# Optimization experiments

Hardware: AMD Instinct MI355X
Metric: run time of the kernel (lower is better)

Reference implementation:

```python
import jax, jax.numpy as jnp
import numpy as np

B, LQ, C = 4, 4096, 384
NH, NL, NP = 6, 1, 4
HL, WL = 64, 64
LV = HL * WL
DH = C // NH
EPS = 1e-6


def layer_norm(x, g, b):
    mu = jnp.mean(x, axis=-1, keepdims=True)
    var = jnp.mean(jnp.square(x - mu), axis=-1, keepdims=True)
    return (x - mu) * jax.lax.rsqrt(var + EPS) * g + b


def ms_deform_attn_core(value, spatial_shapes, level_start_index, loc, attn_w):
    # value [B,LV,NH,DH]; loc [B,LQ,NH,NL,NP,2] in [0,1]; attn_w [B,LQ,NH,NL,NP]
    ss = np.asarray(spatial_shapes)
    lsi = np.asarray(level_start_index)
    Bv, _, nH, dh = value.shape
    Lq = loc.shape[1]
    nP = loc.shape[4]
    out = jnp.zeros((Bv, Lq, nH, dh), value.dtype)
    for l in range(loc.shape[3]):
        Hl, Wl = int(ss[l, 0]), int(ss[l, 1])
        st = int(lsi[l])
        vflat = value[:, st:st + Hl * Wl]  # [B, Hl*Wl, nH, dh]
        xy = loc[:, :, :, l]               # [B,LQ,nH,NP,2]
        # grid_sample(align_corners=False): pixel = loc * size - 0.5
        x = xy[..., 0] * Wl - 0.5
        y = xy[..., 1] * Hl - 0.5
        x0 = jnp.floor(x)
        y0 = jnp.floor(y)
        wx = x - x0
        wy = y - y0
        x0i = x0.astype(jnp.int32)
        y0i = y0.astype(jnp.int32)

        def gather(xi, yi):
            # zero padding outside the feature map (padding_mode='zeros')
            valid = (xi >= 0) & (xi < Wl) & (yi >= 0) & (yi < Hl)
            idx = jnp.clip(yi, 0, Hl - 1) * Wl + jnp.clip(xi, 0, Wl - 1)  # [B,LQ,nH,NP]
            idx2 = idx.transpose(0, 1, 3, 2).reshape(Bv, Lq * nP, nH)
            g = jnp.take_along_axis(vflat, idx2[..., None], axis=1)       # [B,LQ*NP,nH,dh]
            g = g.reshape(Bv, Lq, nP, nH, dh).transpose(0, 1, 3, 2, 4)    # [B,LQ,nH,NP,dh]
            return g * valid[..., None].astype(value.dtype)

        samp = (gather(x0i, y0i) * ((1 - wx) * (1 - wy))[..., None]
                + gather(x0i + 1, y0i) * (wx * (1 - wy))[..., None]
                + gather(x0i, y0i + 1) * ((1 - wx) * wy)[..., None]
                + gather(x0i + 1, y0i + 1) * (wx * wy)[..., None])
        out = out + jnp.einsum('bqhpd,bqhp->bqhd', samp, attn_w[:, :, :, l])
    return out.reshape(Bv, Lq, nH * dh)


def setup_inputs() -> dict:
    key = jax.random.key(0)
    ks = jax.random.split(key, 12)
    s = 0.02
    return {
        'query': jax.random.normal(ks[0], (B, LQ, C), jnp.float32),
        'reference_points': jax.random.uniform(ks[1], (B, LQ, NL, 2), dtype=jnp.float32),
        'feat': jax.random.normal(ks[2], (B, LV, C), jnp.float32),
        'spatial_shapes': jnp.array([[HL, WL]], jnp.int32),
        'level_start_index': jnp.array([0], jnp.int32),
        'ln_q_g': jnp.ones((C,), jnp.float32), 'ln_q_b': jnp.zeros((C,), jnp.float32),
        'ln_f_g': jnp.ones((C,), jnp.float32), 'ln_f_b': jnp.zeros((C,), jnp.float32),
        'gamma': jax.random.normal(ks[3], (C,), jnp.float32) * 0.1,
        'Wv': jax.random.normal(ks[4], (C, C), jnp.float32) * s,
        'bv': jnp.zeros((C,), jnp.float32),
        'Wo': jax.random.normal(ks[5], (C, NH * NL * NP * 2), jnp.float32) * s,
        'bo': jax.random.normal(ks[6], (NH * NL * NP * 2,), jnp.float32) * 0.5,
        'Wa': jax.random.normal(ks[7], (C, NH * NL * NP), jnp.float32) * s,
        'ba': jnp.zeros((NH * NL * NP,), jnp.float32),
        'Wout': jax.random.normal(ks[8], (C, C), jnp.float32) * s,
        'bout': jnp.zeros((C,), jnp.float32),
    }


def reference(query, reference_points, feat, spatial_shapes, level_start_index,
              ln_q_g, ln_q_b, ln_f_g, ln_f_b, gamma,
              Wv, bv, Wo, bo, Wa, ba, Wout, bout):
    q = layer_norm(query, ln_q_g, ln_q_b)
    f = layer_norm(feat, ln_f_g, ln_f_b)
    value = (f @ Wv + bv).reshape(B, LV, NH, DH)
    offsets = (q @ Wo + bo).reshape(B, LQ, NH, NL, NP, 2)
    attn_w = jax.nn.softmax((q @ Wa + ba).reshape(B, LQ, NH, NL * NP), axis=-1)
    attn_w = attn_w.reshape(B, LQ, NH, NL, NP)
    # offset normalizer is (W, H) per level
    norm = jnp.stack([spatial_shapes[:, 1], spatial_shapes[:, 0]], -1).astype(jnp.float32)
    loc = reference_points[:, :, None, :, None, :] + offsets / norm[None, None, None, :, None, :]
    attn = ms_deform_attn_core(value, spatial_shapes, level_start_index, loc, attn_w)
    attn = attn @ Wout + bout
    return query + gamma * attn
```

## Files before the change

kernel.cpp:

```cpp
#include <hip/hip_runtime.h>
#include <math.h>

#define B_    4
#define LQ_   4096
#define C_    384
#define NH_   6
#define NP_   4
#define HL_   64
#define WL_   64
#define LV_   (HL_ * WL_)
#define ROWS_ (B_ * LQ_)
#define EPS_  1e-6f
#define NOFF_ 48
#define NLOG_ 24
#define WCTR_ 128

typedef unsigned short u16;
typedef unsigned int   u32;
typedef __bf16 bf16x8 __attribute__((ext_vector_type(8)));
typedef float  f32x4  __attribute__((ext_vector_type(4)));

__device__ __forceinline__ u16 f2bf(float f) {
    u32 u = __float_as_uint(f);
    u += 0x7fff + ((u >> 16) & 1);
    return (u16)(u >> 16);
}
__device__ __forceinline__ u32 pack2bf(float a, float b) {
    return (u32)f2bf(a) | ((u32)f2bf(b) << 16);
}

__device__ __forceinline__ f32x4 mfma16(bf16x8 a, bf16x8 b, f32x4 c) {
    return __builtin_amdgcn_mfma_f32_16x16x32_bf16(a, b, c, 0, 0, 0);
}

__device__ __forceinline__ void gl_lds16(const u16* g, u16* l) {
    __builtin_amdgcn_global_load_lds(
        (const __attribute__((address_space(1))) unsigned int*)g,
        (__attribute__((address_space(3))) unsigned int*)l, 16, 0, 0);
}

__device__ __forceinline__ void vm_wait4() { asm volatile("s_waitcnt vmcnt(4)" ::: "memory"); }
__device__ __forceinline__ void vm_wait0() { asm volatile("s_waitcnt vmcnt(0)" ::: "memory"); }
__device__ __forceinline__ void lgkm0()    { asm volatile("s_waitcnt lgkmcnt(0)" ::: "memory"); }
__device__ __forceinline__ void barrier_() { asm volatile("s_barrier" ::: "memory"); }

#define LN_BLOCKS_   8192
#define PREP_BLOCKS_ 1345

__global__ __launch_bounds__(256) void ln_prep(
    const float* __restrict__ query, const float* __restrict__ feat,
    const float* __restrict__ qg, const float* __restrict__ qbv,
    const float* __restrict__ fg, const float* __restrict__ fbv,
    u16* __restrict__ qout, u16* __restrict__ fout,
    const float* __restrict__ Wv, const float* __restrict__ Wout,
    const float* __restrict__ Wo, const float* __restrict__ Wa,
    const float* __restrict__ bo, const float* __restrict__ ba,
    u16* __restrict__ WvT, u16* __restrict__ WoutT, u16* __restrict__ WcT,
    float* __restrict__ bias_c)
{
    if (blockIdx.x < LN_BLOCKS_) {
        int wid  = threadIdx.x >> 6;
        int lane = threadIdx.x & 63;
        int row  = blockIdx.x * 4 + wid;
        const float *src, *g, *bsh;
        u16* dst;
        int r;
        if (row < ROWS_) { src = query; g = qg; bsh = qbv; dst = qout; r = row; }
        else             { src = feat;  g = fg; bsh = fbv; dst = fout; r = row - ROWS_; }

        const float* x = src + (size_t)r * C_;
        float4 a4 = *(const float4*)(x + 4 * lane);
        float2 a2 = *(const float2*)(x + 256 + 2 * lane);
        float v0 = a4.x, v1 = a4.y, v2 = a4.z, v3 = a4.w, v4 = a2.x, v5 = a2.y;

        float s = v0 + v1 + v2 + v3 + v4 + v5;
#pragma unroll
        for (int off = 32; off; off >>= 1) s += __shfl_xor(s, off);
        float mu = s * (1.f / C_);

        float d0 = v0 - mu, d1 = v1 - mu, d2 = v2 - mu;
        float d3 = v3 - mu, d4 = v4 - mu, d5 = v5 - mu;
        float s2 = d0*d0 + d1*d1 + d2*d2 + d3*d3 + d4*d4 + d5*d5;
#pragma unroll
        for (int off = 32; off; off >>= 1) s2 += __shfl_xor(s2, off);
        float rs = rsqrtf(s2 * (1.f / C_) + EPS_);

        float4 g4 = *(const float4*)(g + 4 * lane);
        float4 b4 = *(const float4*)(bsh + 4 * lane);
        float2 g2 = *(const float2*)(g + 256 + 2 * lane);
        float2 b2 = *(const float2*)(bsh + 256 + 2 * lane);

        float o0 = d0 * rs * g4.x + b4.x;
        float o1 = d1 * rs * g4.y + b4.y;
        float o2 = d2 * rs * g4.z + b4.z;
        float o3 = d3 * rs * g4.w + b4.w;
        float o4 = d4 * rs * g2.x + b2.x;
        float o5 = d5 * rs * g2.y + b2.y;

        u16* y = dst + (size_t)r * C_;
        uint2 w0; w0.x = pack2bf(o0, o1); w0.y = pack2bf(o2, o3);
        *(uint2*)(y + 4 * lane) = w0;
        *(u32*)(y + 256 + 2 * lane) = pack2bf(o4, o5);
    } else {
        const int KN = 384 * 384;
        int idx = (blockIdx.x - LN_BLOCKS_) * 256 + threadIdx.x;
        if (idx < KN) {
            int n = idx / 384, k = idx - n * 384;
            WvT[idx] = f2bf(Wv[k * 384 + n]);
        } else if (idx < 2 * KN) {
            int t = idx - KN;
            int n = t / 384, k = t - n * 384;
            WoutT[t] = f2bf(Wout[k * 384 + n]);
        } else if (idx < 2 * KN + WCTR_ * 384) {
            int t = idx - 2 * KN;
            int n = t / 384, k = t - n * 384;
            float v = (n < 48) ? Wo[k * 48 + n] : (n < 72 ? Wa[k * 24 + (n - 48)] : 0.f);
            WcT[t] = f2bf(v);
        } else if (idx < 2 * KN + WCTR_ * 384 + 80) {
            int n = idx - (2 * KN + WCTR_ * 384);
            bias_c[n] = (n < 48) ? bo[n] : (n < 72 ? ba[n - 48] : 0.f);
        }
    }
}

__global__ __launch_bounds__(256) void gemm_combined(
    const u16* __restrict__ fb, const u16* __restrict__ qb,
    const u16* __restrict__ WvT, const u16* __restrict__ WcT,
    const float* __restrict__ bv, const float* __restrict__ bias_c,
    u16* __restrict__ valb, float* __restrict__ offs, float* __restrict__ logits)
{
    __shared__ __align__(16) u16 As_[2][4096];
    __shared__ __align__(16) u16 Bs_[2][4096];

    int g    = blockIdx.x;
    int tid  = threadIdx.x;
    int lane = tid & 63, wid = tid >> 6;
    int fr = lane & 15, quad = lane >> 4;

    int srow = tid >> 2;
    int scol = (tid & 3) * 8;

    if (g < 384) {
        int m0 = (g & 127) * 128, n0 = (g >> 7) * 128;
        const u16* aSrc = fb  + (size_t)(m0 + srow) * 384 + scol;
        const u16* bSrc = WvT + (size_t)(n0 + srow) * 384 + scol;

        int wm = (wid >> 1) * 64, wn = (wid & 1) * 64;

        f32x4 zero = {0.f, 0.f, 0.f, 0.f};
        f32x4 acc[4][4];
#pragma unroll
        for (int i = 0; i < 4; ++i)
#pragma unroll
            for (int j = 0; j < 4; ++j) acc[i][j] = zero;

#define STGV(bu, t) { \
            gl_lds16(aSrc + (t)*32,            &As_[bu][tid*8]); \
            gl_lds16(aSrc + 64*384 + (t)*32,   &As_[bu][tid*8 + 2048]); \
            gl_lds16(bSrc + (t)*32,            &Bs_[bu][tid*8]); \
            gl_lds16(bSrc + 64*384 + (t)*32,   &Bs_[bu][tid*8 + 2048]); }

        STGV(0, 0)
        STGV(1, 1)
#pragma unroll
        for (int t = 0; t < 12; ++t) {
            const int bu = t & 1;
            if (t < 11) vm_wait4(); else vm_wait0();
            barrier_();
            bf16x8 af[4], bfr[4];
#pragma unroll
            for (int i = 0; i < 4; ++i) {
                af[i]  = *(const bf16x8*)&As_[bu][(wm + i * 16 + fr) * 32 + quad * 8];
                bfr[i] = *(const bf16x8*)&Bs_[bu][(wn + i * 16 + fr) * 32 + quad * 8];
            }
            lgkm0();
            barrier_();
            if (t < 10) STGV(bu, t + 2)
#pragma unroll
            for (int i = 0; i < 4; ++i)
#pragma unroll
                for (int j = 0; j < 4; ++j)
                    acc[i][j] = mfma16(af[i], bfr[j], acc[i][j]);
        }
#undef STGV

#pragma unroll
        for (int i = 0; i < 4; ++i) {
            int row = m0 + wm + i * 16 + quad * 4;
#pragma unroll
            for (int j = 0; j < 4; ++j) {
                int col = n0 + wn + j * 16 + fr;
                float bcol = bv[col];
#pragma unroll
                for (int r = 0; r < 4; ++r)
                    valb[(size_t)(row + r) * C_ + col] = f2bf(acc[i][j][r] + bcol);
            }
        }
    } else {
        int m0 = (g - 384) * 128;
        const u16* aSrc = qb  + (size_t)(m0 + srow) * 384 + scol;
        const u16* bSrc = WcT + (size_t)srow * 384 + scol;

        int wm = wid * 32;

        f32x4 zero = {0.f, 0.f, 0.f, 0.f};
        f32x4 acc[2][5];
#pragma unroll
        for (int i = 0; i < 2; ++i)
#pragma unroll
            for (int j = 0; j < 5; ++j) acc[i][j] = zero;

#define STGS(bu, t) { \
            gl_lds16(aSrc + (t)*32,            &As_[bu][tid*8]); \
            gl_lds16(aSrc + 64*384 + (t)*32,   &As_[bu][tid*8 + 2048]); \
            gl_lds16(bSrc + (t)*32,            &Bs_[bu][tid*8]); \
            gl_lds16(bSrc + 64*384 + (t)*32,   &Bs_[bu][tid*8 + 2048]); }

        STGS(0, 0)
        STGS(1, 1)
#pragma unroll
        for (int t = 0; t < 12; ++t) {
            const int bu = t & 1;
            if (t < 11) vm_wait4(); else vm_wait0();
            barrier_();
            bf16x8 af[2], bfr[5];
#pragma unroll
            for (int i = 0; i < 2; ++i)
                af[i] = *(const bf16x8*)&As_[bu][(wm + i * 16 + fr) * 32 + quad * 8];
#pragma unroll
            for (int j = 0; j < 5; ++j)
                bfr[j] = *(const bf16x8*)&Bs_[bu][(j * 16 + fr) * 32 + quad * 8];
            lgkm0();
            barrier_();
            if (t < 10) STGS(bu, t + 2)
#pragma unroll
            for (int i = 0; i < 2; ++i)
#pragma unroll
                for (int j = 0; j < 5; ++j)
                    acc[i][j] = mfma16(af[i], bfr[j], acc[i][j]);
        }
#undef STGS

#pragma unroll
        for (int i = 0; i < 2; ++i) {
            int row = m0 + wm + i * 16 + quad * 4;
#pragma unroll
            for (int j = 0; j < 5; ++j) {
                int col = j * 16 + fr;
                if (col < 72) {
                    float bcol = bias_c[col];
#pragma unroll
                    for (int r = 0; r < 4; ++r) {
                        float v = acc[i][j][r] + bcol;
                        if (col < 48) offs[(size_t)(row + r) * NOFF_ + col] = v;
                        else          logits[(size_t)(row + r) * NLOG_ + (col - 48)] = v;
                    }
                }
            }
        }
    }
}

__global__ __launch_bounds__(384) void sampler(
    const u16*  __restrict__ value,
    const float* __restrict__ rp,
    const float* __restrict__ offs,
    const float* __restrict__ logits,
    u16* __restrict__ attn)
{
    int t = threadIdx.x;
    int g = blockIdx.x;
    int b     = (g & 7) >> 1;
    int local = ((g >> 3) << 1) | (g & 1);
    int q  = t / 48, dc = t - q * 48;
    int h  = dc >> 3;
    int col0 = dc << 3;
    int r  = b * LQ_ + local * 8 + q;

    float4 lg  = *(const float4*)(logits + (size_t)r * NLOG_ + h * 4);
    float2 rpv = *(const float2*)(rp + (size_t)r * 2);
    float4 of0 = *(const float4*)(offs + (size_t)r * NOFF_ + h * 8);
    float4 of1 = *(const float4*)(offs + (size_t)r * NOFF_ + h * 8 + 4);

    float mx = fmaxf(fmaxf(lg.x, lg.y), fmaxf(lg.z, lg.w));
    float e0 = __expf(lg.x - mx), e1 = __expf(lg.y - mx);
    float e2 = __expf(lg.z - mx), e3 = __expf(lg.w - mx);
    float rden = 1.f / (e0 + e1 + e2 + e3);
    float aws[4] = {e0 * rden, e1 * rden, e2 * rden, e3 * rden};
    float oxs[4] = {of0.x, of0.z, of1.x, of1.z};
    float oys[4] = {of0.y, of0.w, of1.y, of1.w};

    const u16* vbase = value + (size_t)b * LV_ * C_ + col0;
    float acc[8] = {0.f, 0.f, 0.f, 0.f, 0.f, 0.f, 0.f, 0.f};
#pragma unroll
    for (int p = 0; p < NP_; ++p) {
        float x = rpv.x * (float)WL_ + oxs[p] - 0.5f;
        float y = rpv.y * (float)HL_ + oys[p] - 0.5f;
        float x0f = floorf(x), y0f = floorf(y);
        float wx = x - x0f, wy = y - y0f;
        int x0 = (int)x0f, y0 = (int)y0f;
#pragma unroll
        for (int c = 0; c < 4; ++c) {
            int xi = x0 + (c & 1);
            int yi = y0 + (c >> 1);
            bool valid = (xi >= 0) && (xi < WL_) && (yi >= 0) && (yi < HL_);
            int xc = xi < 0 ? 0 : (xi > WL_ - 1 ? WL_ - 1 : xi);
            int yc = yi < 0 ? 0 : (yi > HL_ - 1 ? HL_ - 1 : yi);
            float w = ((c & 1) ? wx : 1.f - wx) * ((c >> 1) ? wy : 1.f - wy) * aws[p];
            w = valid ? w : 0.f;
            bf16x8 vv = *(const bf16x8*)(vbase + (size_t)(yc * WL_ + xc) * C_);
#pragma unroll
            for (int e = 0; e < 8; ++e) acc[e] += w * (float)vv[e];
        }
    }

    uint4 o;
    o.x = pack2bf(acc[0], acc[1]);
    o.y = pack2bf(acc[2], acc[3]);
    o.z = pack2bf(acc[4], acc[5]);
    o.w = pack2bf(acc[6], acc[7]);
    *(uint4*)(attn + (size_t)r * C_ + col0) = o;
}

__global__ __launch_bounds__(256) void out_gemm(
    const u16* __restrict__ A, const u16* __restrict__ Bt,
    const float* __restrict__ bout, const float* __restrict__ gamma,
    const float* __restrict__ query, float* __restrict__ out)
{
    __shared__ __align__(16) u16 As_[2][4096];
    __shared__ __align__(16) u16 Bs_[2][4096];

    int g    = blockIdx.x;
    int tid  = threadIdx.x;
    int lane = tid & 63, wid = tid >> 6;
    int fr = lane & 15, quad = lane >> 4;

    int srow = tid >> 2;
    int scol = (tid & 3) * 8;

    int m0 = (g & 127) * 128, n0 = (g >> 7) * 96;
    const u16* aSrc = A  + (size_t)(m0 + srow) * 384 + scol;
    const u16* bSrc = Bt + (size_t)(n0 + srow) * 384 + scol;

    int wm = (wid >> 1) * 64, wn = (wid & 1) * 48;

    f32x4 zero = {0.f, 0.f, 0.f, 0.f};
    f32x4 acc[4][3];
#pragma unroll
    for (int i = 0; i < 4; ++i)
#pragma unroll
        for (int j = 0; j < 3; ++j) acc[i][j] = zero;

#define STGO(bu, t) { \
        gl_lds16(aSrc + (t)*32,            &As_[bu][tid*8]); \
        gl_lds16(aSrc + 64*384 + (t)*32,   &As_[bu][tid*8 + 2048]); \
        gl_lds16(bSrc + (t)*32,            &Bs_[bu][tid*8]); \
        gl_lds16(bSrc + 64*384 + (t)*32,   &Bs_[bu][tid*8 + 2048]); }

    STGO(0, 0)
    STGO(1, 1)
#pragma unroll
    for (int t = 0; t < 12; ++t) {
        const int bu = t & 1;
        if (t < 11) vm_wait4(); else vm_wait0();
        barrier_();
        bf16x8 af[4], bfr[3];
#pragma unroll
        for (int i = 0; i < 4; ++i)
            af[i] = *(const bf16x8*)&As_[bu][(wm + i * 16 + fr) * 32 + quad * 8];
#pragma unroll
        for (int j = 0; j < 3; ++j)
            bfr[j] = *(const bf16x8*)&Bs_[bu][(wn + j * 16 + fr) * 32 + quad * 8];
        lgkm0();
        barrier_();
        if (t < 10) STGO(bu, t + 2)
#pragma unroll
        for (int i = 0; i < 4; ++i)
#pragma unroll
            for (int j = 0; j < 3; ++j)
                acc[i][j] = mfma16(af[i], bfr[j], acc[i][j]);
    }
#undef STGO

#pragma unroll
    for (int i = 0; i < 4; ++i) {
        int row = m0 + wm + i * 16 + quad * 4;
#pragma unroll
        for (int j = 0; j < 3; ++j) {
            int col = n0 + wn + j * 16 + fr;
            float bc = bout[col], gm = gamma[col];
#pragma unroll
            for (int r = 0; r < 4; ++r) {
                size_t o = (size_t)(row + r) * C_ + col;
                out[o] = query[o] + gm * (acc[i][j][r] + bc);
            }
        }
    }
}

extern "C" void kernel_launch(void* const* d_in, const int* in_sizes, int n_in,
                              void* d_out, int out_size, void* d_ws, size_t ws_size,
                              hipStream_t stream)
{
    const float* query  = (const float*)d_in[0];
    const float* rp     = (const float*)d_in[1];
    const float* feat   = (const float*)d_in[2];
    const float* gamma  = (const float*)d_in[9];
    const float* Wv     = (const float*)d_in[10];
    const float* bv     = (const float*)d_in[11];
    const float* Wo     = (const float*)d_in[12];
    const float* bo     = (const float*)d_in[13];
    const float* Wa     = (const float*)d_in[14];
    const float* ba     = (const float*)d_in[15];
    const float* Wout   = (const float*)d_in[16];
    const float* bout   = (const float*)d_in[17];
    float* out = (float*)d_out;

    u16* wsu    = (u16*)d_ws;
    u16* qb     = wsu;
    u16* fb     = qb    + (size_t)ROWS_ * C_;
    u16* valb   = fb    + (size_t)ROWS_ * C_;
    u16* attnb  = valb  + (size_t)ROWS_ * C_;
    u16* WvT    = attnb + (size_t)ROWS_ * C_;
    u16* WoutT  = WvT   + 384 * 384;
    u16* WcT    = WoutT + 512 * 384;
    float* offs   = (float*)(WcT + WCTR_ * 384);
    float* logits = offs + (size_t)ROWS_ * NOFF_;
    float* bias_c = logits + (size_t)ROWS_ * NLOG_;

    ln_prep<<<LN_BLOCKS_ + PREP_BLOCKS_, 256, 0, stream>>>(
        query, feat,
        (const float*)d_in[5], (const float*)d_in[6],
        (const float*)d_in[7], (const float*)d_in[8],
        qb, fb, Wv, Wout, Wo, Wa, bo, ba, WvT, WoutT, WcT, bias_c);

    gemm_combined<<<512, 256, 0, stream>>>(fb, qb, WvT, WcT, bv, bias_c,
                                           valb, offs, logits);

    sampler<<<2048, 384, 0, stream>>>(valb, rp, offs, logits, attnb);

    out_gemm<<<512, 256, 0, stream>>>(attnb, WoutT, bout, gamma, query, out);
}
```

Before: 176.9 us.

## Load GEMM fragments straight from global into registers, dropping LDS staging

The three bf16 MFMA GEMMs no longer stage A and B tiles through LDS with global_load_lds and barriers. Each wave now loads its own MFMA fragments directly from global memory into registers, double-buffered one K-step ahead. The aim is to remove the barrier and LDS round-trip cost and to shrink padded weight buffers (WCTR 128 to 80, WoutT offset). The trade-off is that waves sharing a tile now fetch the same data repeatedly from global/L2 with less coalesced 16-byte row loads, and more registers are used.

```diff
diff --git a/kernel.cpp b/kernel.cpp
--- a/kernel.cpp
+++ b/kernel.cpp
@@ -13,7 +13,7 @@
 #define EPS_  1e-6f
 #define NOFF_ 48
 #define NLOG_ 24
-#define WCTR_ 128
+#define WCTR_ 80
 
 typedef unsigned short u16;
 typedef unsigned int   u32;
@@ -33,19 +33,8 @@
     return __builtin_amdgcn_mfma_f32_16x16x32_bf16(a, b, c, 0, 0, 0);
 }
 
-__device__ __forceinline__ void gl_lds16(const u16* g, u16* l) {
-    __builtin_amdgcn_global_load_lds(
-        (const __attribute__((address_space(1))) unsigned int*)g,
-        (__attribute__((address_space(3))) unsigned int*)l, 16, 0, 0);
-}
-
-__device__ __forceinline__ void vm_wait4() { asm volatile("s_waitcnt vmcnt(4)" ::: "memory"); }
-__device__ __forceinline__ void vm_wait0() { asm volatile("s_waitcnt vmcnt(0)" ::: "memory"); }
-__device__ __forceinline__ void lgkm0()    { asm volatile("s_waitcnt lgkmcnt(0)" ::: "memory"); }
-__device__ __forceinline__ void barrier_() { asm volatile("s_barrier" ::: "memory"); }
-
 #define LN_BLOCKS_   8192
-#define PREP_BLOCKS_ 1345
+#define PREP_BLOCKS_ 1273
 
 __global__ __launch_bounds__(256) void ln_prep(
     const float* __restrict__ query, const float* __restrict__ feat,
@@ -129,23 +118,16 @@
     const float* __restrict__ bv, const float* __restrict__ bias_c,
     u16* __restrict__ valb, float* __restrict__ offs, float* __restrict__ logits)
 {
-    __shared__ __align__(16) u16 As_[2][4096];
-    __shared__ __align__(16) u16 Bs_[2][4096];
-
     int g    = blockIdx.x;
     int tid  = threadIdx.x;
     int lane = tid & 63, wid = tid >> 6;
     int fr = lane & 15, quad = lane >> 4;
 
-    int srow = tid >> 2;
-    int scol = (tid & 3) * 8;
-
     if (g < 384) {
         int m0 = (g & 127) * 128, n0 = (g >> 7) * 128;
-        const u16* aSrc = fb  + (size_t)(m0 + srow) * 384 + scol;
-        const u16* bSrc = WvT + (size_t)(n0 + srow) * 384 + scol;
-
         int wm = (wid >> 1) * 64, wn = (wid & 1) * 64;
+        const u16* aBase = fb  + (size_t)(m0 + wm + fr) * 384 + quad * 8;
+        const u16* bBase = WvT + (size_t)(n0 + wn + fr) * 384 + quad * 8;
 
         f32x4 zero = {0.f, 0.f, 0.f, 0.f};
         f32x4 acc[4][4];
@@ -154,35 +136,28 @@
 #pragma unroll
             for (int j = 0; j < 4; ++j) acc[i][j] = zero;
 
-#define STGV(bu, t) { \
-            gl_lds16(aSrc + (t)*32,            &As_[bu][tid*8]); \
-            gl_lds16(aSrc + 64*384 + (t)*32,   &As_[bu][tid*8 + 2048]); \
-            gl_lds16(bSrc + (t)*32,            &Bs_[bu][tid*8]); \
-            gl_lds16(bSrc + 64*384 + (t)*32,   &Bs_[bu][tid*8 + 2048]); }
-
-        STGV(0, 0)
-        STGV(1, 1)
+        bf16x8 af[2][4], bf[2][4];
+#pragma unroll
+        for (int i = 0; i < 4; ++i) {
+            af[0][i] = *(const bf16x8*)(aBase + (size_t)i * 16 * 384);
+            bf[0][i] = *(const bf16x8*)(bBase + (size_t)i * 16 * 384);
+        }
 #pragma unroll
         for (int t = 0; t < 12; ++t) {
-            const int bu = t & 1;
-            if (t < 11) vm_wait4(); else vm_wait0();
-            barrier_();
-            bf16x8 af[4], bfr[4];
-#pragma unroll
-            for (int i = 0; i < 4; ++i) {
-                af[i]  = *(const bf16x8*)&As_[bu][(wm + i * 16 + fr) * 32 + quad * 8];
-                bfr[i] = *(const bf16x8*)&Bs_[bu][(wn + i * 16 + fr) * 32 + quad * 8];
-            }
-            lgkm0();
-            barrier_();
-            if (t < 10) STGV(bu, t + 2)
+            const int cur = t & 1, nxt = cur ^ 1;
+            if (t < 11) {
+#pragma unroll
+                for (int i = 0; i < 4; ++i) {
+                    af[nxt][i] = *(const bf16x8*)(aBase + (size_t)i * 16 * 384 + (t + 1) * 32);
+                    bf[nxt][i] = *(const bf16x8*)(bBase + (size_t)i * 16 * 384 + (t + 1) * 32);
+                }
+            }
 #pragma unroll
             for (int i = 0; i < 4; ++i)
 #pragma unroll
                 for (int j = 0; j < 4; ++j)
-                    acc[i][j] = mfma16(af[i], bfr[j], acc[i][j]);
-        }
-#undef STGV
+                    acc[i][j] = mfma16(af[cur][i], bf[cur][j], acc[i][j]);
+        }
 
 #pragma unroll
         for (int i = 0; i < 4; ++i) {
@@ -198,10 +173,9 @@
         }
     } else {
         int m0 = (g - 384) * 128;
-        const u16* aSrc = qb  + (size_t)(m0 + srow) * 384 + scol;
-        const u16* bSrc = WcT + (size_t)srow * 384 + scol;
-
         int wm = wid * 32;
+        const u16* aBase = qb  + (size_t)(m0 + wm + fr) * 384 + quad * 8;
+        const u16* bBase = WcT + (size_t)fr * 384 + quad * 8;
 
         f32x4 zero = {0.f, 0.f, 0.f, 0.f};
         f32x4 acc[2][5];
@@ -210,36 +184,30 @@
 #pragma unroll
             for (int j = 0; j < 5; ++j) acc[i][j] = zero;
 
-#define STGS(bu, t) { \
-            gl_lds16(aSrc + (t)*32,            &As_[bu][tid*8]); \
-            gl_lds16(aSrc + 64*384 + (t)*32,   &As_[bu][tid*8 + 2048]); \
-            gl_lds16(bSrc + (t)*32,            &Bs_[bu][tid*8]); \
-            gl_lds16(bSrc + 64*384 + (t)*32,   &Bs_[bu][tid*8 + 2048]); }
-
-        STGS(0, 0)
-        STGS(1, 1)
+        bf16x8 af[2][2], bf[2][5];
+#pragma unroll
+        for (int i = 0; i < 2; ++i)
+            af[0][i] = *(const bf16x8*)(aBase + (size_t)i * 16 * 384);
+#pragma unroll
+        for (int j = 0; j < 5; ++j)
+            bf[0][j] = *(const bf16x8*)(bBase + (size_t)j * 16 * 384);
 #pragma unroll
         for (int t = 0; t < 12; ++t) {
-            const int bu = t & 1;
-            if (t < 11) vm_wait4(); else vm_wait0();
-            barrier_();
-            bf16x8 af[2], bfr[5];
+            const int cur = t & 1, nxt = cur ^ 1;
+            if (t < 11) {
+#pragma unroll
+                for (int i = 0; i < 2; ++i)
+                    af[nxt][i] = *(const bf16x8*)(aBase + (size_t)i * 16 * 384 + (t + 1) * 32);
+#pragma unroll
+                for (int j = 0; j < 5; ++j)
+                    bf[nxt][j] = *(const bf16x8*)(bBase + (size_t)j * 16 * 384 + (t + 1) * 32);
+            }
 #pragma unroll
             for (int i = 0; i < 2; ++i)
-                af[i] = *(const bf16x8*)&As_[bu][(wm + i * 16 + fr) * 32 + quad * 8];
-#pragma unroll
-            for (int j = 0; j < 5; ++j)
-                bfr[j] = *(const bf16x8*)&Bs_[bu][(j * 16 + fr) * 32 + quad * 8];
-            lgkm0();
-            barrier_();
-            if (t < 10) STGS(bu, t + 2)
-#pragma unroll
-            for (int i = 0; i < 2; ++i)
 #pragma unroll
                 for (int j = 0; j < 5; ++j)
-                    acc[i][j] = mfma16(af[i], bfr[j], acc[i][j]);
-        }
-#undef STGS
+                    acc[i][j] = mfma16(af[cur][i], bf[cur][j], acc[i][j]);
+        }
 
 #pragma unroll
         for (int i = 0; i < 2; ++i) {
@@ -327,22 +295,15 @@
     const float* __restrict__ bout, const float* __restrict__ gamma,
     const float* __restrict__ query, float* __restrict__ out)
 {
-    __shared__ __align__(16) u16 As_[2][4096];
-    __shared__ __align__(16) u16 Bs_[2][4096];
-
     int g    = blockIdx.x;
     int tid  = threadIdx.x;
     int lane = tid & 63, wid = tid >> 6;
     int fr = lane & 15, quad = lane >> 4;
 
-    int srow = tid >> 2;
-    int scol = (tid & 3) * 8;
-
     int m0 = (g & 127) * 128, n0 = (g >> 7) * 96;
-    const u16* aSrc = A  + (size_t)(m0 + srow) * 384 + scol;
-    const u16* bSrc = Bt + (size_t)(n0 + srow) * 384 + scol;
-
     int wm = (wid >> 1) * 64, wn = (wid & 1) * 48;
+    const u16* aBase = A  + (size_t)(m0 + wm + fr) * 384 + quad * 8;
+    const u16* bBase = Bt + (size_t)(n0 + wn + fr) * 384 + quad * 8;
 
     f32x4 zero = {0.f, 0.f, 0.f, 0.f};
     f32x4 acc[4][3];
@@ -351,36 +312,30 @@
 #pragma unroll
         for (int j = 0; j < 3; ++j) acc[i][j] = zero;
 
-#define STGO(bu, t) { \
-        gl_lds16(aSrc + (t)*32,            &As_[bu][tid*8]); \
-        gl_lds16(aSrc + 64*384 + (t)*32,   &As_[bu][tid*8 + 2048]); \
-        gl_lds16(bSrc + (t)*32,            &Bs_[bu][tid*8]); \
-        gl_lds16(bSrc + 64*384 + (t)*32,   &Bs_[bu][tid*8 + 2048]); }
-
-    STGO(0, 0)
-    STGO(1, 1)
+    bf16x8 af[2][4], bf[2][3];
+#pragma unroll
+    for (int i = 0; i < 4; ++i)
+        af[0][i] = *(const bf16x8*)(aBase + (size_t)i * 16 * 384);
+#pragma unroll
+    for (int j = 0; j < 3; ++j)
+        bf[0][j] = *(const bf16x8*)(bBase + (size_t)j * 16 * 384);
 #pragma unroll
     for (int t = 0; t < 12; ++t) {
-        const int bu = t & 1;
-        if (t < 11) vm_wait4(); else vm_wait0();
-        barrier_();
-        bf16x8 af[4], bfr[3];
+        const int cur = t & 1, nxt = cur ^ 1;
+        if (t < 11) {
+#pragma unroll
+            for (int i = 0; i < 4; ++i)
+                af[nxt][i] = *(const bf16x8*)(aBase + (size_t)i * 16 * 384 + (t + 1) * 32);
+#pragma unroll
+            for (int j = 0; j < 3; ++j)
+                bf[nxt][j] = *(const bf16x8*)(bBase + (size_t)j * 16 * 384 + (t + 1) * 32);
+        }
 #pragma unroll
         for (int i = 0; i < 4; ++i)
-            af[i] = *(const bf16x8*)&As_[bu][(wm + i * 16 + fr) * 32 + quad * 8];
-#pragma unroll
-        for (int j = 0; j < 3; ++j)
-            bfr[j] = *(const bf16x8*)&Bs_[bu][(wn + j * 16 + fr) * 32 + quad * 8];
-        lgkm0();
-        barrier_();
-        if (t < 10) STGO(bu, t + 2)
-#pragma unroll
-        for (int i = 0; i < 4; ++i)
 #pragma unroll
             for (int j = 0; j < 3; ++j)
-                acc[i][j] = mfma16(af[i], bfr[j], acc[i][j]);
-    }
-#undef STGO
+                acc[i][j] = mfma16(af[cur][i], bf[cur][j], acc[i][j]);
+    }
 
 #pragma unroll
     for (int i = 0; i < 4; ++i) {
@@ -423,7 +378,7 @@
     u16* attnb  = valb  + (size_t)ROWS_ * C_;
     u16* WvT    = attnb + (size_t)ROWS_ * C_;
     u16* WoutT  = WvT   + 384 * 384;
-    u16* WcT    = WoutT + 512 * 384;
+    u16* WcT    = WoutT + 384 * 384;
     float* offs   = (float*)(WcT + WCTR_ * 384);
     float* logits = offs + (size_t)ROWS_ * NOFF_;
     float* bias_c = logits + (size_t)ROWS_ * NLOG_;
```

After: 196.6 us. 11.1% more time.
